# Optimization experiments

Hardware: AMD Instinct MI355X
Metric: run time of the kernel (lower is better)

Reference implementation:

```python
import jax, jax.numpy as jnp
import numpy as np

N, K, C = 100000, 32, 128  # n_nodes, max_degree, channels


def setup_inputs() -> dict:
    key = jax.random.key(0)
    k1, k2, k3, k4 = jax.random.split(key, 4)
    x = jax.random.normal(k1, (N, C), dtype=jnp.float32)
    edge_index = jax.random.randint(k2, (N, K), 0, N, dtype=jnp.int64)
    # GCNConv uses nn.Linear(in, out, bias=False): weight shape [out, in]
    W1 = jax.random.normal(k3, (C, C), dtype=jnp.float32) / np.sqrt(C)
    W2 = jax.random.normal(k4, (C, C), dtype=jnp.float32) / np.sqrt(C)
    return {"x": x, "edge_index": edge_index, "W1": W1, "W2": W2}


def _gcn_layer(x, edge_index, W):
    # node degree counts valid (>=0) neighbors plus self
    deg = jnp.sum(edge_index >= 0, axis=-1, keepdims=True).astype(x.dtype) + 1.0
    sqrt_deg = jnp.sqrt(deg)
    h = (x @ W.T) / sqrt_deg  # [N, C]
    # pad with a zero row so index -1 (padding) gathers zeros
    padded = jnp.concatenate([h, jnp.zeros((1, h.shape[-1]), h.dtype)], axis=0)
    neigh_sum = padded[edge_index].sum(axis=1)  # [N, K, C] -> [N, C]
    return (neigh_sum + h) / sqrt_deg


def reference(x, edge_index, W1, W2):
    h = jax.nn.elu(_gcn_layer(x, edge_index, W1))
    h = jax.nn.elu(_gcn_layer(h, edge_index, W2))
    return h
```

## Files before the change

kernel.cpp:

```cpp
#include <hip/hip_runtime.h>
#include <hip/hip_bf16.h>
#include <math.h>

namespace {

constexpr int C = 128;
constexpr int K = 32;

typedef float float4v __attribute__((ext_vector_type(4)));
typedef short short8v __attribute__((ext_vector_type(8)));
typedef unsigned short ushort8v __attribute__((ext_vector_type(8)));
typedef int int2v __attribute__((ext_vector_type(2)));

__device__ __forceinline__ float bf2f(unsigned short u) {
    return __uint_as_float(((unsigned int)u) << 16);
}
__device__ __forceinline__ unsigned short f2bf(float x) {
    __hip_bfloat16 h = __float2bfloat16(x);
    return *(unsigned short*)&h;
}

__global__ __launch_bounds__(256) void deg_kernel(
    const int* __restrict__ edge, float* __restrict__ invs,
    unsigned int* __restrict__ hz1, unsigned int* __restrict__ hz2,
    const float* __restrict__ W1, const float* __restrict__ W2,
    unsigned short* __restrict__ whl, int N) {
    const int bid = blockIdx.x;
    const int t = threadIdx.x;

    if (bid == 0 && t < 64) hz1[(size_t)N * (C / 2) + t] = 0u;
    if (bid == 129 && t < 64) hz2[(size_t)N * (C / 2) + t] = 0u;
    if (bid >= 1 && bid <= 128) {
        int which = (bid - 1) >> 6;
        int p = ((bid - 1) & 63) * 256 + t;
        float w = (which ? W2 : W1)[p];
        unsigned short hb = f2bf(w);
        unsigned short lb = f2bf(w - bf2f(hb));
        unsigned short* dst = whl + (size_t)which * 32768;
        dst[p] = hb;
        dst[16384 + p] = lb;
    }

    int node = bid * 32 + (t >> 3);
    int k4 = (t & 7) * 4;
    int4 e = make_int4(-1, -1, -1, -1);
    if (node < N) e = *(const int4*)(edge + (size_t)node * K + k4);
    int cnt = (e.x >= 0) + (e.y >= 0) + (e.z >= 0) + (e.w >= 0);
    cnt += __shfl_xor(cnt, 1);
    cnt += __shfl_xor(cnt, 2);
    cnt += __shfl_xor(cnt, 4);
    if ((t & 7) == 0 && node < N)
        invs[node] = 1.0f / sqrtf((float)(cnt + 1));
}

__global__ __launch_bounds__(256, 2) void gemm_mfma_kernel(
    const float* __restrict__ X, const unsigned short* __restrict__ Wp,
    const float* __restrict__ invs, unsigned short* __restrict__ H, int N) {
    __shared__ unsigned short Whl[2][C][136];

    const int t = threadIdx.x;
    const int n0 = blockIdx.x * 128;

    for (int p = t; p < 2 * C * 16; p += 256) {
        int seg = p >> 11;
        int rem = p & 2047;
        int row = rem >> 4;
        int v8 = (rem & 15) * 8;
        *(ushort8v*)&Whl[seg][row][v8] =
            *(const ushort8v*)(Wp + (size_t)seg * 16384 + row * 128 + v8);
    }
    __syncthreads();

    const int wv = t >> 6;
    const int l = t & 63;
    const int lm = l & 15;
    const int lk = l >> 4;
    const int rbase = n0 + wv * 32;

    int rowA0 = rbase + lm;
    int rowA1 = rbase + 16 + lm;
    rowA0 = rowA0 < N ? rowA0 : N - 1;
    rowA1 = rowA1 < N ? rowA1 : N - 1;
    const float* xp0 = X + (size_t)rowA0 * C;
    const float* xp1 = X + (size_t)rowA1 * C;

    float4v acc[2][8];
#pragma unroll
    for (int rt = 0; rt < 2; ++rt)
#pragma unroll
        for (int ct = 0; ct < 8; ++ct) acc[rt][ct] = {0.f, 0.f, 0.f, 0.f};

#pragma unroll
    for (int ks = 0; ks < 4; ++ks) {
        const int kb = ks * 32 + lk * 8;
        float xr0[8], xr1[8];
        *(float4v*)&xr0[0] = *(const float4v*)(xp0 + kb);
        *(float4v*)&xr0[4] = *(const float4v*)(xp0 + kb + 4);
        *(float4v*)&xr1[0] = *(const float4v*)(xp1 + kb);
        *(float4v*)&xr1[4] = *(const float4v*)(xp1 + kb + 4);
        short8v ah0, al0, ah1, al1;
#pragma unroll
        for (int j = 0; j < 8; ++j) {
            unsigned short h0 = f2bf(xr0[j]);
            unsigned short h1 = f2bf(xr1[j]);
            ah0[j] = (short)h0;
            ah1[j] = (short)h1;
            al0[j] = (short)f2bf(xr0[j] - bf2f(h0));
            al1[j] = (short)f2bf(xr1[j] - bf2f(h1));
        }
#pragma unroll
        for (int ct = 0; ct < 8; ++ct) {
            short8v bh = *(const short8v*)&Whl[0][ct * 16 + lm][kb];
            short8v bl = *(const short8v*)&Whl[1][ct * 16 + lm][kb];
            acc[0][ct] = __builtin_amdgcn_mfma_f32_16x16x32_bf16(ah0, bh,
                                                                 acc[0][ct], 0, 0, 0);
            acc[0][ct] = __builtin_amdgcn_mfma_f32_16x16x32_bf16(al0, bh,
                                                                 acc[0][ct], 0, 0, 0);
            acc[0][ct] = __builtin_amdgcn_mfma_f32_16x16x32_bf16(ah0, bl,
                                                                 acc[0][ct], 0, 0, 0);
            acc[1][ct] = __builtin_amdgcn_mfma_f32_16x16x32_bf16(ah1, bh,
                                                                 acc[1][ct], 0, 0, 0);
            acc[1][ct] = __builtin_amdgcn_mfma_f32_16x16x32_bf16(al1, bh,
                                                                 acc[1][ct], 0, 0, 0);
            acc[1][ct] = __builtin_amdgcn_mfma_f32_16x16x32_bf16(ah1, bl,
                                                                 acc[1][ct], 0, 0, 0);
        }
    }

    float sc[2][4];
#pragma unroll
    for (int rt = 0; rt < 2; ++rt)
#pragma unroll
        for (int q = 0; q < 4; ++q) {
            int r = rbase + rt * 16 + lk * 4 + q;
            sc[rt][q] = invs[r < N ? r : N - 1];
        }
#pragma unroll
    for (int rt = 0; rt < 2; ++rt)
#pragma unroll
        for (int ct = 0; ct < 8; ++ct)
#pragma unroll
            for (int q = 0; q < 4; ++q) {
                int r = rbase + rt * 16 + lk * 4 + q;
                if (r < N)
                    H[(size_t)r * C + ct * 16 + lm] =
                        f2bf(acc[rt][ct][q] * sc[rt][q]);
            }
}

__global__ __launch_bounds__(256) void gather_elu_kernel(
    const unsigned short* __restrict__ H, const int* __restrict__ edge,
    const float* __restrict__ invs, float* __restrict__ out, int N) {
    __shared__ int idx_s[16][K];

    const int t = threadIdx.x;
    const int g = t >> 4;
    const int l16 = t & 15;
    const int node = blockIdx.x * 16 + g;

    {
        int p = t * 2;
        int r = p >> 5;
        int c0 = p & 31;
        int nn = blockIdx.x * 16 + r;
        int2v e = {-1, -1};
        if (nn < N) e = *(const int2v*)(edge + (size_t)nn * K + c0);
        idx_s[r][c0] = e.x;
        idx_s[r][c0 + 1] = e.y;
    }
    __syncthreads();
    if (node >= N) return;

    const unsigned short* hp = H + l16 * 8;
    float acc[8];
#pragma unroll
    for (int i = 0; i < 8; ++i) acc[i] = 0.f;

#pragma unroll
    for (int k0 = 0; k0 < K; k0 += 16) {
        ushort8v v[16];
#pragma unroll
        for (int u = 0; u < 16; ++u) {
            int j = idx_s[g][k0 + u];
            j = (j < 0) ? N : j;
            v[u] = *(const ushort8v*)(hp + (size_t)j * C);
        }
#pragma unroll
        for (int u = 0; u < 16; ++u)
#pragma unroll
            for (int i = 0; i < 8; ++i) acc[i] += bf2f(v[u][i]);
    }

    ushort8v sv = *(const ushort8v*)(hp + (size_t)node * C);
    float s = invs[node];
    float r[8];
#pragma unroll
    for (int i = 0; i < 8; ++i) {
        float x = (acc[i] + bf2f(sv[i])) * s;
        r[i] = x > 0.f ? x : expm1f(x);
    }
    float* dst = out + (size_t)node * C + l16 * 8;
    float4v lo = {r[0], r[1], r[2], r[3]};
    float4v hi = {r[4], r[5], r[6], r[7]};
    *(float4v*)dst = lo;
    *(float4v*)(dst + 4) = hi;
}

__global__ __launch_bounds__(256) void fused_gather_gemm_kernel(
    const unsigned short* __restrict__ H1, const int* __restrict__ edge,
    const float* __restrict__ invs, const float* __restrict__ W2,
    unsigned short* __restrict__ H2, int N) {
    __shared__ unsigned short Whl[2][C][136];
    __shared__ unsigned short act_s[16][136];
    __shared__ int idx_s[16][K];

    const int t = threadIdx.x;
    const int base = blockIdx.x * 16;

    for (int p = t; p < C * 32; p += 256) {
        int row = p >> 5;
        int c4 = (p & 31) * 4;
        float4 w = ((const float4*)W2)[p];
        float wv[4] = {w.x, w.y, w.z, w.w};
#pragma unroll
        for (int j = 0; j < 4; ++j) {
            unsigned short hb = f2bf(wv[j]);
            Whl[0][row][c4 + j] = hb;
            Whl[1][row][c4 + j] = f2bf(wv[j] - bf2f(hb));
        }
    }
    {
        int p = t * 2;
        int r = p >> 5;
        int c0 = p & 31;
        int nn = base + r;
        int2v e = {-1, -1};
        if (nn < N) e = *(const int2v*)(edge + (size_t)nn * K + c0);
        idx_s[r][c0] = e.x;
        idx_s[r][c0 + 1] = e.y;
    }
    __syncthreads();

    {
        const int g = t >> 4;
        const int l16 = t & 15;
        const int node = base + g;
        const unsigned short* hp = H1 + l16 * 8;
        float acc[8];
#pragma unroll
        for (int i = 0; i < 8; ++i) acc[i] = 0.f;

#pragma unroll
        for (int k0 = 0; k0 < K; k0 += 16) {
            ushort8v v[16];
#pragma unroll
            for (int u = 0; u < 16; ++u) {
                int j = idx_s[g][k0 + u];
                j = (j < 0) ? N : j;
                v[u] = *(const ushort8v*)(hp + (size_t)j * C);
            }
#pragma unroll
            for (int u = 0; u < 16; ++u)
#pragma unroll
                for (int i = 0; i < 8; ++i) acc[i] += bf2f(v[u][i]);
        }

        ushort8v av = {0, 0, 0, 0, 0, 0, 0, 0};
        if (node < N) {
            ushort8v sv = *(const ushort8v*)(hp + (size_t)node * C);
            float s = invs[node];
#pragma unroll
            for (int i = 0; i < 8; ++i) {
                float x = (acc[i] + bf2f(sv[i])) * s;
                x = x > 0.f ? x : expm1f(x);
                av[i] = f2bf(x);
            }
        }
        *(ushort8v*)&act_s[g][l16 * 8] = av;
    }
    __syncthreads();

    const int wv = t >> 6;
    const int l = t & 63;
    const int lm = l & 15;
    const int lk = l >> 4;

    float4v o[2] = {{0.f, 0.f, 0.f, 0.f}, {0.f, 0.f, 0.f, 0.f}};
#pragma unroll
    for (int ks = 0; ks < 4; ++ks) {
        const int kb = ks * 32 + lk * 8;
        short8v a = *(const short8v*)&act_s[lm][kb];
#pragma unroll
        for (int ci = 0; ci < 2; ++ci) {
            const int ct = wv * 2 + ci;
            short8v bh = *(const short8v*)&Whl[0][ct * 16 + lm][kb];
            short8v bl = *(const short8v*)&Whl[1][ct * 16 + lm][kb];
            o[ci] = __builtin_amdgcn_mfma_f32_16x16x32_bf16(a, bh, o[ci], 0, 0, 0);
            o[ci] = __builtin_amdgcn_mfma_f32_16x16x32_bf16(a, bl, o[ci], 0, 0, 0);
        }
    }

#pragma unroll
    for (int q = 0; q < 4; ++q) {
        const int nd = base + lk * 4 + q;
        if (nd < N) {
            float s = invs[nd];
#pragma unroll
            for (int ci = 0; ci < 2; ++ci) {
                H2[(size_t)nd * C + (wv * 2 + ci) * 16 + lm] =
                    f2bf(o[ci][q] * s);
            }
        }
    }
}

}

extern "C" void kernel_launch(void* const* d_in, const int* in_sizes, int n_in,
                              void* d_out, int out_size, void* d_ws, size_t ws_size,
                              hipStream_t stream) {
    const float* x = (const float*)d_in[0];
    const int* edge = (const int*)d_in[1];
    const float* W1 = (const float*)d_in[2];
    const float* W2 = (const float*)d_in[3];
    float* out = (float*)d_out;
    const int N = in_sizes[0] / C;

    char* ws = (char*)d_ws;
    const size_t invs_bytes = ((size_t)N * sizeof(float) + 255) & ~(size_t)255;
    const size_t h_bytes = (((size_t)(N + 1) * C * 2) + 255) & ~(size_t)255;
    const size_t whl_bytes = 2 * 2 * 16384 * sizeof(unsigned short);

    float* invs = (float*)ws;
    unsigned short* h1 = (unsigned short*)(ws + invs_bytes);

    const int degBlocks = (N + 31) / 32;
    const int gemmBlocks = (N + 127) / 128;
    const int gatherBlocks = (N + 15) / 16;

    if (ws_size >= invs_bytes + 2 * h_bytes + whl_bytes) {
        unsigned short* h2 = (unsigned short*)(ws + invs_bytes + h_bytes);
        unsigned short* whl = (unsigned short*)(ws + invs_bytes + 2 * h_bytes);

        deg_kernel<<<degBlocks, 256, 0, stream>>>(
            edge, invs, (unsigned int*)h1, (unsigned int*)h2, W1, W2, whl, N);
        gemm_mfma_kernel<<<gemmBlocks, 256, 0, stream>>>(x, whl, invs, h1, N);
        fused_gather_gemm_kernel<<<gatherBlocks, 256, 0, stream>>>(
            h1, edge, invs, W2, h2, N);
        gather_elu_kernel<<<gatherBlocks, 256, 0, stream>>>(h2, edge, invs, out, N);
    } else {
        unsigned short* whl = (unsigned short*)(ws + invs_bytes + h_bytes);

        deg_kernel<<<degBlocks, 256, 0, stream>>>(
            edge, invs, (unsigned int*)h1, (unsigned int*)h1, W1, W2, whl, N);
        gemm_mfma_kernel<<<gemmBlocks, 256, 0, stream>>>(x, whl, invs, h1, N);
        gather_elu_kernel<<<gatherBlocks, 256, 0, stream>>>(h1, edge, invs, out, N);
        gemm_mfma_kernel<<<gemmBlocks, 256, 0, stream>>>(out, whl + 32768, invs,
                                                         h1, N);
        gather_elu_kernel<<<gatherBlocks, 256, 0, stream>>>(h1, edge, invs, out, N);
    }
}
```

Measured before the change: 307.8 us.

## Use pre-split W2 from workspace in registers and widen fused gather block to 512

The fused layer-2 gather+GEMM kernel no longer converts W2 from fp32 into a large shared-memory hi/lo bf16 tile in every block. Each wave now loads its B fragments directly from the pre-split bf16 weights already produced by deg_kernel. The block grows to 512 threads: 32 lanes per node each gather 4 channels, and 8 waves each own one 16-column output tile. This removes the per-block weight conversion and about 70KB of LDS, which should raise occupancy. The costs are narrower 8-byte gather loads and more vector registers holding weight fragments.

```diff
diff --git a/kernel.cpp b/kernel.cpp
--- a/kernel.cpp
+++ b/kernel.cpp
@@ -206,111 +206,92 @@
     *(float4v*)(dst + 4) = hi;
 }
 
-__global__ __launch_bounds__(256) void fused_gather_gemm_kernel(
+__global__ __launch_bounds__(512) void fused_gather_gemm_kernel(
     const unsigned short* __restrict__ H1, const int* __restrict__ edge,
-    const float* __restrict__ invs, const float* __restrict__ W2,
+    const float* __restrict__ invs, const unsigned short* __restrict__ W2p,
     unsigned short* __restrict__ H2, int N) {
-    __shared__ unsigned short Whl[2][C][136];
     __shared__ unsigned short act_s[16][136];
     __shared__ int idx_s[16][K];
 
     const int t = threadIdx.x;
     const int base = blockIdx.x * 16;
 
-    for (int p = t; p < C * 32; p += 256) {
-        int row = p >> 5;
-        int c4 = (p & 31) * 4;
-        float4 w = ((const float4*)W2)[p];
-        float wv[4] = {w.x, w.y, w.z, w.w};
-#pragma unroll
-        for (int j = 0; j < 4; ++j) {
-            unsigned short hb = f2bf(wv[j]);
-            Whl[0][row][c4 + j] = hb;
-            Whl[1][row][c4 + j] = f2bf(wv[j] - bf2f(hb));
-        }
-    }
     {
-        int p = t * 2;
-        int r = p >> 5;
-        int c0 = p & 31;
+        int r = t >> 5, c0 = t & 31;
         int nn = base + r;
-        int2v e = {-1, -1};
-        if (nn < N) e = *(const int2v*)(edge + (size_t)nn * K + c0);
-        idx_s[r][c0] = e.x;
-        idx_s[r][c0 + 1] = e.y;
-    }
-    __syncthreads();
-
-    {
-        const int g = t >> 4;
-        const int l16 = t & 15;
-        const int node = base + g;
-        const unsigned short* hp = H1 + l16 * 8;
-        float acc[8];
-#pragma unroll
-        for (int i = 0; i < 8; ++i) acc[i] = 0.f;
-
-#pragma unroll
-        for (int k0 = 0; k0 < K; k0 += 16) {
-            ushort8v v[16];
-#pragma unroll
-            for (int u = 0; u < 16; ++u) {
-                int j = idx_s[g][k0 + u];
-                j = (j < 0) ? N : j;
-                v[u] = *(const ushort8v*)(hp + (size_t)j * C);
-            }
-#pragma unroll
-            for (int u = 0; u < 16; ++u)
-#pragma unroll
-                for (int i = 0; i < 8; ++i) acc[i] += bf2f(v[u][i]);
-        }
-
-        ushort8v av = {0, 0, 0, 0, 0, 0, 0, 0};
-        if (node < N) {
-            ushort8v sv = *(const ushort8v*)(hp + (size_t)node * C);
-            float s = invs[node];
-#pragma unroll
-            for (int i = 0; i < 8; ++i) {
-                float x = (acc[i] + bf2f(sv[i])) * s;
-                x = x > 0.f ? x : expm1f(x);
-                av[i] = f2bf(x);
-            }
-        }
-        *(ushort8v*)&act_s[g][l16 * 8] = av;
-    }
-    __syncthreads();
+        idx_s[r][c0] = (nn < N) ? edge[(size_t)nn * K + c0] : -1;
+    }
 
     const int wv = t >> 6;
     const int l = t & 63;
     const int lm = l & 15;
     const int lk = l >> 4;
-
-    float4v o[2] = {{0.f, 0.f, 0.f, 0.f}, {0.f, 0.f, 0.f, 0.f}};
+    short8v bfrag[2][4];
+#pragma unroll
+    for (int pl = 0; pl < 2; ++pl)
+#pragma unroll
+        for (int ks = 0; ks < 4; ++ks)
+            bfrag[pl][ks] = *(const short8v*)(W2p + (size_t)pl * 16384 +
+                                              (wv * 16 + lm) * 128 + ks * 32 +
+                                              lk * 8);
+
+    __syncthreads();
+
+    {
+        const int g = t >> 5;
+        const int lane32 = t & 31;
+        const int node = base + g;
+        const unsigned short* hp = H1 + lane32 * 4;
+        float a0 = 0.f, a1 = 0.f, a2 = 0.f, a3 = 0.f;
+
+#pragma unroll
+        for (int k0 = 0; k0 < K; k0 += 16) {
+            ushort4 v[16];
+#pragma unroll
+            for (int u = 0; u < 16; ++u) {
+                int j = idx_s[g][k0 + u];
+                j = (j < 0) ? N : j;
+                v[u] = *(const ushort4*)(hp + (size_t)j * C);
+            }
+#pragma unroll
+            for (int u = 0; u < 16; ++u) {
+                a0 += bf2f(v[u].x);
+                a1 += bf2f(v[u].y);
+                a2 += bf2f(v[u].z);
+                a3 += bf2f(v[u].w);
+            }
+        }
+
+        ushort4 av = {0, 0, 0, 0};
+        if (node < N) {
+            ushort4 sv = *(const ushort4*)(hp + (size_t)node * C);
+            float s = invs[node];
+            float x0 = (a0 + bf2f(sv.x)) * s;
+            float x1 = (a1 + bf2f(sv.y)) * s;
+            float x2 = (a2 + bf2f(sv.z)) * s;
+            float x3 = (a3 + bf2f(sv.w)) * s;
+            av.x = f2bf(x0 > 0.f ? x0 : expm1f(x0));
+            av.y = f2bf(x1 > 0.f ? x1 : expm1f(x1));
+            av.z = f2bf(x2 > 0.f ? x2 : expm1f(x2));
+            av.w = f2bf(x3 > 0.f ? x3 : expm1f(x3));
+        }
+        *(ushort4*)&act_s[g][lane32 * 4] = av;
+    }
+    __syncthreads();
+
+    float4v o = {0.f, 0.f, 0.f, 0.f};
 #pragma unroll
     for (int ks = 0; ks < 4; ++ks) {
-        const int kb = ks * 32 + lk * 8;
-        short8v a = *(const short8v*)&act_s[lm][kb];
-#pragma unroll
-        for (int ci = 0; ci < 2; ++ci) {
-            const int ct = wv * 2 + ci;
-            short8v bh = *(const short8v*)&Whl[0][ct * 16 + lm][kb];
-            short8v bl = *(const short8v*)&Whl[1][ct * 16 + lm][kb];
-            o[ci] = __builtin_amdgcn_mfma_f32_16x16x32_bf16(a, bh, o[ci], 0, 0, 0);
-            o[ci] = __builtin_amdgcn_mfma_f32_16x16x32_bf16(a, bl, o[ci], 0, 0, 0);
-        }
+        short8v a = *(const short8v*)&act_s[lm][ks * 32 + lk * 8];
+        o = __builtin_amdgcn_mfma_f32_16x16x32_bf16(a, bfrag[0][ks], o, 0, 0, 0);
+        o = __builtin_amdgcn_mfma_f32_16x16x32_bf16(a, bfrag[1][ks], o, 0, 0, 0);
     }
 
 #pragma unroll
     for (int q = 0; q < 4; ++q) {
         const int nd = base + lk * 4 + q;
-        if (nd < N) {
-            float s = invs[nd];
-#pragma unroll
-            for (int ci = 0; ci < 2; ++ci) {
-                H2[(size_t)nd * C + (wv * 2 + ci) * 16 + lm] =
-                    f2bf(o[ci][q] * s);
-            }
-        }
+        if (nd < N)
+            H2[(size_t)nd * C + wv * 16 + lm] = f2bf(o[q] * invs[nd]);
     }
 }
 
@@ -345,8 +326,8 @@
         deg_kernel<<<degBlocks, 256, 0, stream>>>(
             edge, invs, (unsigned int*)h1, (unsigned int*)h2, W1, W2, whl, N);
         gemm_mfma_kernel<<<gemmBlocks, 256, 0, stream>>>(x, whl, invs, h1, N);
-        fused_gather_gemm_kernel<<<gatherBlocks, 256, 0, stream>>>(
-            h1, edge, invs, W2, h2, N);
+        fused_gather_gemm_kernel<<<gatherBlocks, 512, 0, stream>>>(
+            h1, edge, invs, whl + 32768, h2, N);
         gather_elu_kernel<<<gatherBlocks, 256, 0, stream>>>(h2, edge, invs, out, N);
     } else {
         unsigned short* whl = (unsigned short*)(ws + invs_bytes + h_bytes);
```

Result: faster. 279.8 us (-9.1%).
